# Kernel tuning notes

Measured on AMD Instinct MI355X. Metric: run time of the kernel, lower is better.

The kernel has to match this reference:

```python
import jax, jax.numpy as jnp
import numpy as np

B, S, D, E, H, K = 2, 2048, 1024, 8, 4096, 2


def setup_inputs() -> dict:
    key = jax.random.key(0)
    ks = jax.random.split(key, 8)
    w = lambda i, shape: jax.random.normal(ks[i], shape, jnp.float32) * 0.02
    return {
        "x": jax.random.normal(ks[0], (B, S, D), jnp.float32),
        "noise": jax.random.normal(ks[1], (B, S, E), jnp.float32),
        "Wg": w(2, (E, D)),
        "noise_weight": jnp.zeros((E,), jnp.float32),
        "W1": w(3, (E, D, H)),
        "b1": jnp.zeros((E, H), jnp.float32),
        "W2": w(4, (E, D, H)),
        "b2": jnp.zeros((E, H), jnp.float32),
        "Wp": w(5, (E, H, D)),
        "bp": jnp.zeros((E, D), jnp.float32),
        "k": K,
    }


def reference(x, noise, Wg, noise_weight, W1, b1, W2, b2, Wp, bp, k):
    Bb, Ss, Dd = x.shape
    Ee = Wg.shape[0]
    # --- noisy top-k gate (noisy_std = 1.0) ---
    logits = jnp.einsum('bsd,ed->bse', x, Wg)
    noisy = logits + noise * noise_weight            # [B,S,E]
    vals, idx = jax.lax.top_k(noisy, k)              # [B,S,k]
    oh = jax.nn.one_hot(idx, Ee, dtype=x.dtype)      # [B,S,k,E]
    sel = oh.sum(axis=-2) > 0                        # [B,S,E] selected mask
    scat = (oh * vals[..., None]).sum(axis=-2)       # scatter topk logits
    sparse = jnp.where(sel, scat, -jnp.inf)
    gate = jax.nn.softmax(sparse, axis=-1)           # zero weight off-topk
    # --- dense-equivalent expert compute (gate==0 off top-k => same math as masked dispatch) ---
    xf = x.reshape(Bb * Ss, Dd)                      # [T,D]
    gf = gate.reshape(Bb * Ss, Ee)                   # [T,E]
    h1 = jnp.einsum('td,edh->eth', xf, W1) + b1[:, None, :]
    h2 = jnp.einsum('td,edh->eth', xf, W2) + b2[:, None, :]
    hh = h1 * jax.nn.silu(h2)                        # SwiGLU
    outs = jnp.einsum('eth,ehd->etd', hh, Wp) + bp[:, None, :]
    final = jnp.einsum('etd,te->td', outs, gf).reshape(Bb, Ss, Dd)
    return final, idx
```

## Files before the change

kernel.cpp:

```cpp
#include <hip/hip_runtime.h>
#include <math.h>

#define Bc 2
#define Sc 2048
#define Dc 1024
#define Ec 8
#define Hc 4096
#define Tc (Bc*Sc)
#define NSLOT (Tc*2)
#define SLOTPAD 8448
#define FINAL_N ((size_t)Tc*Dc)
#define BK 32
#define PROWS ((size_t)SLOTPAD*32)

typedef float f32x4 __attribute__((ext_vector_type(4)));
typedef __bf16 bf16x8 __attribute__((ext_vector_type(8)));

__device__ __forceinline__ unsigned short f2bf(float f) {
    union { float f; unsigned int u; } v; v.f = f;
    return (unsigned short)((v.u + 0x7fffu + ((v.u >> 16) & 1u)) >> 16);
}
__device__ __forceinline__ unsigned int pack2bf(float a, float b) {
    return (unsigned int)f2bf(a) | ((unsigned int)f2bf(b) << 16);
}

__device__ __forceinline__ void gload16(const unsigned short* g, unsigned short* l) {
    __builtin_amdgcn_global_load_lds(
        (const __attribute__((address_space(1))) unsigned int*)g,
        (__attribute__((address_space(3))) unsigned int*)l,
        16, 0, 0);
}

__device__ __forceinline__ void fence_bar() {
    __builtin_amdgcn_sched_barrier(0);
    asm volatile("s_barrier" ::: "memory");
    __builtin_amdgcn_sched_barrier(0);
}

__global__ void k_transpose_panel(const float* __restrict__ inA, const float* __restrict__ inB,
                                  unsigned short* __restrict__ outA, unsigned short* __restrict__ outB,
                                  int R, int C, int nz_per_mat) {
    __shared__ float tile[64][65];
    int z = blockIdx.z;
    const float* in; unsigned short* out;
    if (z < nz_per_mat) { in = inA; out = outA; }
    else { in = inB; out = outB; z -= nz_per_mat; }
    size_t zbase = (size_t)z * (size_t)R * C;
    int R32 = R >> 5;
    int cb = blockIdx.x * 64, rb = blockIdx.y * 64;
    int t = threadIdx.x;
    int q = t & 15, g = t >> 4;
    #pragma unroll
    for (int j = 0; j < 4; j++) {
        int row = g + 16*j;
        float4 v = *(const float4*)&in[zbase + (size_t)(rb+row)*C + cb + q*4];
        tile[row][q*4+0] = v.x; tile[row][q*4+1] = v.y;
        tile[row][q*4+2] = v.z; tile[row][q*4+3] = v.w;
    }
    __syncthreads();
    #pragma unroll
    for (int j = 0; j < 4; j++) {
        int co = g + 16*j;
        int c = cb + co;
        int r0 = rb + q*4;
        ushort4 o;
        o.x = f2bf(tile[q*4+0][co]); o.y = f2bf(tile[q*4+1][co]);
        o.z = f2bf(tile[q*4+2][co]); o.w = f2bf(tile[q*4+3][co]);
        int cr = c & 127;
        int ch = ((r0 >> 3) & 3) ^ ((cr >> 1) & 3);
        size_t off = zbase + (((size_t)(c >> 7) * R32 + (r0 >> 5)) * 4096)
                   + (size_t)cr * 32 + ch * 8 + (r0 & 7);
        *(ushort4*)&out[off] = o;
    }
}

__global__ void k_gate(const float* __restrict__ x, const float* __restrict__ noise,
                       const float* __restrict__ Wg, const float* __restrict__ nw,
                       float* __restrict__ out_idx, int* __restrict__ counts,
                       int* __restrict__ tok_top, float* __restrict__ tok_w) {
    int t = blockIdx.x;
    int lane = threadIdx.x;
    const float* xr = x + (size_t)t * Dc;
    double acc[Ec];
    #pragma unroll
    for (int e = 0; e < Ec; e++) acc[e] = 0.0;
    for (int i = 0; i < Dc/64; i++) {
        int d = lane + i*64;
        double xv = (double)xr[d];
        #pragma unroll
        for (int e = 0; e < Ec; e++) acc[e] += xv * (double)Wg[e*Dc + d];
    }
    #pragma unroll
    for (int e = 0; e < Ec; e++)
        for (int off = 32; off > 0; off >>= 1)
            acc[e] += __shfl_down(acc[e], off);
    if (lane == 0) {
        double noisy[Ec];
        #pragma unroll
        for (int e = 0; e < Ec; e++)
            noisy[e] = acc[e] + (double)noise[t*Ec + e] * (double)nw[e];
        int i0 = 0;
        for (int e = 1; e < Ec; e++) if (noisy[e] > noisy[i0]) i0 = e;
        int i1 = -1;
        for (int e = 0; e < Ec; e++) {
            if (e == i0) continue;
            if (i1 < 0 || noisy[e] > noisy[i1]) i1 = e;
        }
        double ee = exp(noisy[i1] - noisy[i0]);
        float w0 = (float)(1.0 / (1.0 + ee));
        float w1 = (float)(ee / (1.0 + ee));
        out_idx[t*2 + 0] = (float)i0;
        out_idx[t*2 + 1] = (float)i1;
        tok_top[t*2] = i0; tok_top[t*2+1] = i1;
        tok_w[t*2] = w0;   tok_w[t*2+1] = w1;
        atomicAdd(&counts[i0], 1);
        atomicAdd(&counts[i1], 1);
    }
}

__global__ void k_scan(const int* __restrict__ counts, int* __restrict__ offsets) {
    if (threadIdx.x == 0) {
        int s = 0;
        for (int e = 0; e < Ec; e++) { offsets[e] = s; s += counts[e]; }
        offsets[Ec] = s;
    }
}

__global__ void k_fill(const int* __restrict__ tok_top, const int* __restrict__ offsets,
                       int* __restrict__ fill, int* __restrict__ slot_token,
                       int* __restrict__ slot_of, int* __restrict__ slot_pos) {
    int t = blockIdx.x * 256 + threadIdx.x;
    if (t >= Tc) return;
    #pragma unroll
    for (int j = 0; j < 2; j++) {
        int e = tok_top[t*2 + j];
        int pos = atomicAdd(&fill[e], 1);
        int slot = offsets[e] + pos;
        slot_token[slot] = t;
        slot_of[t*2 + j] = slot;
        slot_pos[slot] = pos;
    }
}

__global__ void k_packA(const float* __restrict__ x, const int* __restrict__ slot_token,
                        const int* __restrict__ slot_pos, unsigned short* __restrict__ apk) {
    int s = blockIdx.x * 4 + (threadIdx.x >> 6);
    int lane = threadIdx.x & 63;
    int token = slot_token[s];
    int pos = slot_pos[s];
    const float4* px = (const float4*)(x + (size_t)token * Dc) + lane*4;
    float4 v0 = px[0], v1 = px[1], v2 = px[2], v3 = px[3];
    uint4 lo, hi;
    lo.x = pack2bf(v0.x, v0.y); lo.y = pack2bf(v0.z, v0.w);
    lo.z = pack2bf(v1.x, v1.y); lo.w = pack2bf(v1.z, v1.w);
    hi.x = pack2bf(v2.x, v2.y); hi.y = pack2bf(v2.z, v2.w);
    hi.z = pack2bf(v3.x, v3.y); hi.w = pack2bf(v3.z, v3.w);
    int kp = lane >> 1;
    int key = (pos >> 1) & 3;
    int c0 = (lane & 1) * 2;
    size_t base = (size_t)kp * PROWS + (size_t)s * 32;
    *(uint4*)&apk[base + ((c0 ^ key) * 8)]       = lo;
    *(uint4*)&apk[base + (((c0+1) ^ key) * 8)]   = hi;
}

#define BM1 256
#define BN1 128
#define A1SZ (BM1*BK)
#define W1SZ (BN1*BK)

__global__ __launch_bounds__(512, 2) void k_gemm1(
    const unsigned short* __restrict__ apk,
    const unsigned short* __restrict__ w1p, const unsigned short* __restrict__ w2p,
    const float* __restrict__ b1, const float* __restrict__ b2,
    const int* __restrict__ counts, const int* __restrict__ offsets,
    unsigned short* __restrict__ hh2) {
    int e = blockIdx.z;
    int n_e = counts[e];
    int m0 = blockIdx.y * BM1;
    if (m0 >= n_e) return;
    int base = offsets[e];
    int hp = blockIdx.x;
    int n0 = hp * BN1;

    __shared__ __align__(16) unsigned short sA[3*A1SZ];
    __shared__ __align__(16) unsigned short sW1[3*W1SZ];
    __shared__ __align__(16) unsigned short sW2[3*W1SZ];

    int tid = threadIdx.x;
    int wid = tid >> 6, lane = tid & 63;
    int wr = wid >> 1, wc = wid & 1;

    const unsigned short* pa  = apk + (size_t)(base + m0 + wid*32) * 32 + lane*8;
    const unsigned short* pw1 = w1p + ((size_t)(e*32 + hp) * 32) * 4096 + wid*512 + lane*8;
    const unsigned short* pw2 = w2p + ((size_t)(e*32 + hp) * 32) * 4096 + wid*512 + lane*8;

    f32x4 acc1[4][4], acc2[4][4];
    #pragma unroll
    for (int m = 0; m < 4; m++)
        #pragma unroll
        for (int n = 0; n < 4; n++)
            #pragma unroll
            for (int j = 0; j < 4; j++) { acc1[m][n][j] = 0.0f; acc2[m][n][j] = 0.0f; }

    int arow = lane & 15, cr = lane >> 4;
    int ccf = cr ^ ((arow >> 1) & 3);
    int offA[4], offW[4];
    #pragma unroll
    for (int m = 0; m < 4; m++) offA[m] = (wr*64 + m*16 + arow)*BK + ccf*8;
    #pragma unroll
    for (int n = 0; n < 4; n++) offW[n] = (wc*64 + n*16 + arow)*BK + ccf*8;

    auto STAGE = [&](int buf, int kp) {
        unsigned short* dA = sA + buf*A1SZ + wid*1024;
        const unsigned short* a = pa + (size_t)kp * PROWS;
        gload16(a,       dA);
        gload16(a + 512, dA + 512);
        gload16(pw1 + kp*4096, sW1 + buf*W1SZ + wid*512);
        gload16(pw2 + kp*4096, sW2 + buf*W1SZ + wid*512);
    };

#define LDF1(buf, a, w1f, w2f) { \
    const unsigned short* lA_ = sA  + (buf)*A1SZ; \
    const unsigned short* l1_ = sW1 + (buf)*W1SZ; \
    const unsigned short* l2_ = sW2 + (buf)*W1SZ; \
    _Pragma("unroll") for (int m_ = 0; m_ < 4; m_++) a[m_] = *(const bf16x8*)&lA_[offA[m_]]; \
    _Pragma("unroll") for (int n_ = 0; n_ < 4; n_++) { \
        w1f[n_] = *(const bf16x8*)&l1_[offW[n_]]; \
        w2f[n_] = *(const bf16x8*)&l2_[offW[n_]]; } }

#define MM1(a, w1f, w2f) { \
    _Pragma("unroll") for (int m_ = 0; m_ < 4; m_++) \
        _Pragma("unroll") for (int n_ = 0; n_ < 4; n_++) { \
            acc1[m_][n_] = __builtin_amdgcn_mfma_f32_16x16x32_bf16(a[m_], w1f[n_], acc1[m_][n_], 0, 0, 0); \
            acc2[m_][n_] = __builtin_amdgcn_mfma_f32_16x16x32_bf16(a[m_], w2f[n_], acc2[m_][n_], 0, 0, 0); } }

    bf16x8 a0[4], x10[4], x20[4], a1[4], x11[4], x21[4];

    STAGE(0, 0); STAGE(1, 1);
    asm volatile("s_waitcnt vmcnt(4)" ::: "memory");
    fence_bar();
    LDF1(0, a0, x10, x20);
    asm volatile("s_waitcnt lgkmcnt(0)" ::: "memory");
    __builtin_amdgcn_sched_barrier(0);

    const int NT = Dc / BK;
    int ib = 0;

#define G1ITER(T, CA, CW1, CW2, NA, NW1, NW2) { \
    int i1_ = ib + 1; if (i1_ == 3) i1_ = 0; \
    int i2_ = i1_ + 1; if (i2_ == 3) i2_ = 0; \
    if ((T) + 2 < NT) { \
        STAGE(i2_, (T)+2); \
        asm volatile("s_waitcnt vmcnt(4)" ::: "memory");    \
    } else if ((T) + 1 < NT) { \
        asm volatile("s_waitcnt vmcnt(0)" ::: "memory"); \
    } \
    fence_bar();                                 \
    __builtin_amdgcn_s_setprio(1); \
    if ((T) + 1 < NT) LDF1(i1_, NA, NW1, NW2);   \
    MM1(CA, CW1, CW2); \
    __builtin_amdgcn_s_setprio(0); \
    asm volatile("s_waitcnt lgkmcnt(0)" ::: "memory"); \
    __builtin_amdgcn_sched_barrier(0); \
    ib = i1_; }

    for (int t = 0; t < NT; t += 2) {
        G1ITER(t,   a0, x10, x20, a1, x11, x21);
        G1ITER(t+1, a1, x11, x21, a0, x10, x20);
    }

    int lrow = (lane >> 4) * 4, lcol = lane & 15;
    #pragma unroll
    for (int n = 0; n < 4; n++) {
        int hcol = n0 + wc*64 + n*16 + lcol;
        float bias1 = b1[e*Hc + hcol], bias2 = b2[e*Hc + hcol];
        int hp2 = hcol >> 5;
        int ch  = (hcol >> 3) & 3;
        int ho  = hcol & 7;
        #pragma unroll
        for (int m = 0; m < 4; m++) {
            int rb2 = m0 + wr*64 + m*16 + lrow;
            #pragma unroll
            for (int j = 0; j < 4; j++) {
                int r = rb2 + j;
                if (r < n_e) {
                    float h1v = acc1[m][n][j] + bias1;
                    float h2v = acc2[m][n][j] + bias2;
                    float hhv = h1v * (h2v / (1.0f + expf(-h2v)));
                    int key = (r >> 1) & 3;
                    hh2[(size_t)hp2 * PROWS + (size_t)(base + r)*32 + ((ch ^ key)*8) + ho] = f2bf(hhv);
                }
            }
        }
    }
#undef G1ITER
#undef MM1
#undef LDF1
}

#define BM2 256
#define BN2 128
#define A2SZ (BM2*BK)
#define B2SZ (BN2*BK)

__global__ __launch_bounds__(512, 2) void k_gemm2(
    const unsigned short* __restrict__ hh2,
    const unsigned short* __restrict__ wpp,
    const float* __restrict__ bp,
    const int* __restrict__ counts, const int* __restrict__ offsets,
    float* __restrict__ outb) {
    int e = blockIdx.z;
    int n_e = counts[e];
    int m0 = blockIdx.y * BM2;
    if (m0 >= n_e) return;
    int base = offsets[e];
    int dp = blockIdx.x;
    int n0 = dp * BN2;

    __shared__ __align__(16) unsigned short sA[3*A2SZ];
    __shared__ __align__(16) unsigned short sB[3*B2SZ];

    int tid = threadIdx.x;
    int wid = tid >> 6, lane = tid & 63;
    int wr = wid >> 1, wc = wid & 1;

    const unsigned short* pa = hh2 + (size_t)(base + m0 + wid*32) * 32 + lane*8;
    const unsigned short* pb = wpp + ((size_t)(e*8 + dp) * 128) * 4096 + wid*512 + lane*8;

    f32x4 acc[4][4];
    #pragma unroll
    for (int m = 0; m < 4; m++)
        #pragma unroll
        for (int n = 0; n < 4; n++)
            #pragma unroll
            for (int j = 0; j < 4; j++) acc[m][n][j] = 0.0f;

    int arow = lane & 15, cr = lane >> 4;
    int ccf = cr ^ ((arow >> 1) & 3);
    int offA[4], offW[4];
    #pragma unroll
    for (int m = 0; m < 4; m++) offA[m] = (wr*64 + m*16 + arow)*BK + ccf*8;
    #pragma unroll
    for (int n = 0; n < 4; n++) offW[n] = (wc*64 + n*16 + arow)*BK + ccf*8;

    auto STAGE = [&](int buf, int kp) {
        unsigned short* dA = sA + buf*A2SZ + wid*1024;
        const unsigned short* a = pa + (size_t)kp * PROWS;
        gload16(a,       dA);
        gload16(a + 512, dA + 512);
        gload16(pb + kp*4096, sB + buf*B2SZ + wid*512);
    };

#define LDF2(buf, a, b) { \
    const unsigned short* lA_ = sA + (buf)*A2SZ; \
    const unsigned short* lB_ = sB + (buf)*B2SZ; \
    _Pragma("unroll") for (int m_ = 0; m_ < 4; m_++) a[m_] = *(const bf16x8*)&lA_[offA[m_]]; \
    _Pragma("unroll") for (int n_ = 0; n_ < 4; n_++) b[n_] = *(const bf16x8*)&lB_[offW[n_]]; }

#define MM2(a, b) { \
    _Pragma("unroll") for (int m_ = 0; m_ < 4; m_++) \
        _Pragma("unroll") for (int n_ = 0; n_ < 4; n_++) \
            acc[m_][n_] = __builtin_amdgcn_mfma_f32_16x16x32_bf16(a[m_], b[n_], acc[m_][n_], 0, 0, 0); }

    bf16x8 a0[4], b0[4], a1[4], b1f[4];

    STAGE(0, 0); STAGE(1, 1);
    asm volatile("s_waitcnt vmcnt(3)" ::: "memory");
    fence_bar();
    LDF2(0, a0, b0);
    asm volatile("s_waitcnt lgkmcnt(0)" ::: "memory");
    __builtin_amdgcn_sched_barrier(0);

    const int NT = Hc / BK;
    int ib = 0;

#define G2ITER(T, CA, CB, NA, NB) { \
    int i1_ = ib + 1; if (i1_ == 3) i1_ = 0; \
    int i2_ = i1_ + 1; if (i2_ == 3) i2_ = 0; \
    if ((T) + 2 < NT) { \
        STAGE(i2_, (T)+2); \
        asm volatile("s_waitcnt vmcnt(3)" ::: "memory"); \
    } else if ((T) + 1 < NT) { \
        asm volatile("s_waitcnt vmcnt(0)" ::: "memory"); \
    } \
    fence_bar(); \
    __builtin_amdgcn_s_setprio(1); \
    if ((T) + 1 < NT) LDF2(i1_, NA, NB); \
    MM2(CA, CB); \
    __builtin_amdgcn_s_setprio(0); \
    asm volatile("s_waitcnt lgkmcnt(0)" ::: "memory"); \
    __builtin_amdgcn_sched_barrier(0); \
    ib = i1_; }

    for (int t = 0; t < NT; t += 2) {
        G2ITER(t,   a0, b0, a1, b1f);
        G2ITER(t+1, a1, b1f, a0, b0);
    }

    int lrow = (lane >> 4) * 4, lcol = lane & 15;
    #pragma unroll
    for (int n = 0; n < 4; n++) {
        int dcol = n0 + wc*64 + n*16 + lcol;
        float bias = bp[e*Dc + dcol];
        #pragma unroll
        for (int m = 0; m < 4; m++) {
            int rb2 = m0 + wr*64 + m*16 + lrow;
            #pragma unroll
            for (int j = 0; j < 4; j++) {
                int r = rb2 + j;
                if (r < n_e)
                    outb[(size_t)(base + r)*Dc + dcol] = acc[m][n][j] + bias;
            }
        }
    }
#undef G2ITER
#undef MM2
#undef LDF2
}

__global__ void k_combine(const float* __restrict__ outb, const int* __restrict__ slot_of,
                          const float* __restrict__ tok_w, float* __restrict__ final_out) {
    int gid = blockIdx.x * 256 + threadIdx.x;
    int t = gid >> 8;
    int c = (gid & 255) * 4;
    int s0 = slot_of[t*2], s1 = slot_of[t*2 + 1];
    float w0 = tok_w[t*2], w1 = tok_w[t*2 + 1];
    float4 o0 = *(const float4*)&outb[(size_t)s0*Dc + c];
    float4 o1 = *(const float4*)&outb[(size_t)s1*Dc + c];
    float4 r;
    r.x = w0*o0.x + w1*o1.x;
    r.y = w0*o0.y + w1*o1.y;
    r.z = w0*o0.z + w1*o1.z;
    r.w = w0*o0.w + w1*o1.w;
    *(float4*)&final_out[(size_t)t*Dc + c] = r;
}

extern "C" void kernel_launch(void* const* d_in, const int* in_sizes, int n_in,
                              void* d_out, int out_size, void* d_ws, size_t ws_size,
                              hipStream_t stream) {
    (void)in_sizes; (void)n_in; (void)out_size; (void)ws_size;
    const float* x     = (const float*)d_in[0];
    const float* noise = (const float*)d_in[1];
    const float* Wg    = (const float*)d_in[2];
    const float* nw    = (const float*)d_in[3];
    const float* W1    = (const float*)d_in[4];
    const float* b1    = (const float*)d_in[5];
    const float* W2    = (const float*)d_in[6];
    const float* b2    = (const float*)d_in[7];
    const float* Wp    = (const float*)d_in[8];
    const float* bp    = (const float*)d_in[9];

    char* ws = (char*)d_ws;
    size_t off = 0;
    unsigned short* W1P = (unsigned short*)(ws + off); off += (size_t)Ec*Dc*Hc*2;
    unsigned short* W2P = (unsigned short*)(ws + off); off += (size_t)Ec*Dc*Hc*2;
    unsigned short* WPP = (unsigned short*)(ws + off); off += (size_t)Ec*Hc*Dc*2;
    unsigned short* APK = (unsigned short*)(ws + off); off += (size_t)32*PROWS*2;
    unsigned short* HH2 = (unsigned short*)(ws + off); off += (size_t)128*PROWS*2;
    float*          OUTB= (float*)(ws + off);          off += (size_t)NSLOT*Dc*4;
    int*   counts    = (int*)(ws + off);
    int*   fill      = (int*)(ws + off + 32);
    int*   offsets   = (int*)(ws + off + 64);
    int*   tok_top   = (int*)(ws + off + 128);
    float* tok_w     = (float*)(ws + off + 128 + (size_t)Tc*2*4);
    int*   slot_token= (int*)(ws + off + 128 + (size_t)Tc*2*8);
    int*   slot_of   = (int*)(ws + off + 128 + (size_t)Tc*2*8 + (size_t)NSLOT*4);
    int*   slot_pos  = (int*)(ws + off + 128 + (size_t)Tc*2*8 + (size_t)NSLOT*8);

    float* final_out = (float*)d_out;
    float* idx_out   = (float*)d_out + FINAL_N;

    hipMemsetAsync(counts, 0, 64, stream);

    k_transpose_panel<<<dim3(Hc/64, Dc/64, 2*Ec), 256, 0, stream>>>(W1, W2, W1P, W2P, Dc, Hc, Ec);
    k_transpose_panel<<<dim3(Dc/64, Hc/64, Ec), 256, 0, stream>>>(Wp, Wp, WPP, WPP, Hc, Dc, Ec);

    k_gate<<<Tc, 64, 0, stream>>>(x, noise, Wg, nw, idx_out, counts, tok_top, tok_w);
    k_scan<<<1, 64, 0, stream>>>(counts, offsets);
    k_fill<<<Tc/256, 256, 0, stream>>>(tok_top, offsets, fill, slot_token, slot_of, slot_pos);
    k_packA<<<NSLOT/4, 256, 0, stream>>>(x, slot_token, slot_pos, APK);

    k_gemm1<<<dim3(Hc/BN1, Tc/BM1, Ec), 512, 0, stream>>>(APK, W1P, W2P, b1, b2,
                                                          counts, offsets, HH2);
    k_gemm2<<<dim3(Dc/BN2, Tc/BM2, Ec), 512, 0, stream>>>(HH2, WPP, bp, counts, offsets, OUTB);
    k_combine<<<(Tc*Dc/4)/256, 256, 0, stream>>>(OUTB, slot_of, tok_w, final_out);
}
```

Before: 696.9 us.

## Restructure expert GEMM mainloops to BK=64 stages with interleaved sub-phase loads

Both grouped expert GEMMs now stage 64-wide K tiles (two 32-wide panels) per pipeline step. Each step is split into sub-phases that interleave LDS fragment reads, async global-to-LDS loads and MFMA bursts. gemm1 moves to a double-buffered 4x2 wave layout in which each wave covers 128 rows by 32 columns, so only four A fragments are held at a time, lowering register pressure. gemm2 keeps a three-stage ring at the larger K depth. The aim is fewer barriers per unit of K and better overlap of loads with MFMA work; in exchange it adds more fence barriers per step and more LDS, which may hurt occupancy.

```diff
diff --git a/kernel.cpp b/kernel.cpp
--- a/kernel.cpp
+++ b/kernel.cpp
@@ -10,8 +10,9 @@
 #define NSLOT (Tc*2)
 #define SLOTPAD 8448
 #define FINAL_N ((size_t)Tc*Dc)
-#define BK 32
 #define PROWS ((size_t)SLOTPAD*32)
+#define NKT1 16
+#define NKT2 64
 
 typedef float f32x4 __attribute__((ext_vector_type(4)));
 typedef __bf16 bf16x8 __attribute__((ext_vector_type(8)));
@@ -163,11 +164,6 @@
     *(uint4*)&apk[base + (((c0+1) ^ key) * 8)]   = hi;
 }
 
-#define BM1 256
-#define BN1 128
-#define A1SZ (BM1*BK)
-#define W1SZ (BN1*BK)
-
 __global__ __launch_bounds__(512, 2) void k_gemm1(
     const unsigned short* __restrict__ apk,
     const unsigned short* __restrict__ w1p, const unsigned short* __restrict__ w2p,
@@ -176,116 +172,122 @@
     unsigned short* __restrict__ hh2) {
     int e = blockIdx.z;
     int n_e = counts[e];
-    int m0 = blockIdx.y * BM1;
+    int m0 = blockIdx.y * 256;
     if (m0 >= n_e) return;
     int base = offsets[e];
     int hp = blockIdx.x;
-    int n0 = hp * BN1;
-
-    __shared__ __align__(16) unsigned short sA[3*A1SZ];
-    __shared__ __align__(16) unsigned short sW1[3*W1SZ];
-    __shared__ __align__(16) unsigned short sW2[3*W1SZ];
+    int n0 = hp * 128;
+
+    __shared__ __align__(16) unsigned short sA[2][2][8192];
+    __shared__ __align__(16) unsigned short sW1[2][8192];
+    __shared__ __align__(16) unsigned short sW2[2][8192];
 
     int tid = threadIdx.x;
     int wid = tid >> 6, lane = tid & 63;
-    int wr = wid >> 1, wc = wid & 1;
-
-    const unsigned short* pa  = apk + (size_t)(base + m0 + wid*32) * 32 + lane*8;
-    const unsigned short* pw1 = w1p + ((size_t)(e*32 + hp) * 32) * 4096 + wid*512 + lane*8;
-    const unsigned short* pw2 = w2p + ((size_t)(e*32 + hp) * 32) * 4096 + wid*512 + lane*8;
-
-    f32x4 acc1[4][4], acc2[4][4];
-    #pragma unroll
-    for (int m = 0; m < 4; m++)
-        #pragma unroll
-        for (int n = 0; n < 4; n++)
-            #pragma unroll
-            for (int j = 0; j < 4; j++) { acc1[m][n][j] = 0.0f; acc2[m][n][j] = 0.0f; }
+    int wr = wid >> 2, wc = wid & 3;
+
+    const unsigned short* aSrc  = apk + (size_t)(base + m0 + wid*32)*32 + lane*8;
+    const size_t wOff = (size_t)(e*32 + hp) * 32 * 4096;
+    const unsigned short* w1Src = w1p + wOff + wid*1024 + lane*8;
+    const unsigned short* w2Src = w2p + wOff + wid*1024 + lane*8;
 
     int arow = lane & 15, cr = lane >> 4;
     int ccf = cr ^ ((arow >> 1) & 3);
-    int offA[4], offW[4];
-    #pragma unroll
-    for (int m = 0; m < 4; m++) offA[m] = (wr*64 + m*16 + arow)*BK + ccf*8;
-    #pragma unroll
-    for (int n = 0; n < 4; n++) offW[n] = (wc*64 + n*16 + arow)*BK + ccf*8;
-
-    auto STAGE = [&](int buf, int kp) {
-        unsigned short* dA = sA + buf*A1SZ + wid*1024;
-        const unsigned short* a = pa + (size_t)kp * PROWS;
-        gload16(a,       dA);
-        gload16(a + 512, dA + 512);
-        gload16(pw1 + kp*4096, sW1 + buf*W1SZ + wid*512);
-        gload16(pw2 + kp*4096, sW2 + buf*W1SZ + wid*512);
+    int aoff[8], woff[2];
+    #pragma unroll
+    for (int rf = 0; rf < 8; rf++) aoff[rf] = (wr*128 + rf*16 + arow)*32 + ccf*8;
+    #pragma unroll
+    for (int cf = 0; cf < 2; cf++) woff[cf] = (wc*32 + cf*16 + arow)*32 + ccf*8;
+
+    f32x4 acc1[8][2], acc2[8][2];
+    #pragma unroll
+    for (int rf = 0; rf < 8; rf++)
+        #pragma unroll
+        for (int cf = 0; cf < 2; cf++)
+            #pragma unroll
+            for (int j = 0; j < 4; j++) { acc1[rf][cf][j] = 0.0f; acc2[rf][cf][j] = 0.0f; }
+
+    bf16x8 af[4], w1f[2], w2f[2];
+
+    auto ST_W1 = [&](int ss, int kt) {
+        const unsigned short* s_ = w1Src + (size_t)kt*8192;
+        unsigned short* d_ = &sW1[ss][0] + wid*1024;
+        gload16(s_, d_); gload16(s_ + 512, d_ + 512);
     };
-
-#define LDF1(buf, a, w1f, w2f) { \
-    const unsigned short* lA_ = sA  + (buf)*A1SZ; \
-    const unsigned short* l1_ = sW1 + (buf)*W1SZ; \
-    const unsigned short* l2_ = sW2 + (buf)*W1SZ; \
-    _Pragma("unroll") for (int m_ = 0; m_ < 4; m_++) a[m_] = *(const bf16x8*)&lA_[offA[m_]]; \
-    _Pragma("unroll") for (int n_ = 0; n_ < 4; n_++) { \
-        w1f[n_] = *(const bf16x8*)&l1_[offW[n_]]; \
-        w2f[n_] = *(const bf16x8*)&l2_[offW[n_]]; } }
-
-#define MM1(a, w1f, w2f) { \
-    _Pragma("unroll") for (int m_ = 0; m_ < 4; m_++) \
-        _Pragma("unroll") for (int n_ = 0; n_ < 4; n_++) { \
-            acc1[m_][n_] = __builtin_amdgcn_mfma_f32_16x16x32_bf16(a[m_], w1f[n_], acc1[m_][n_], 0, 0, 0); \
-            acc2[m_][n_] = __builtin_amdgcn_mfma_f32_16x16x32_bf16(a[m_], w2f[n_], acc2[m_][n_], 0, 0, 0); } }
-
-    bf16x8 a0[4], x10[4], x20[4], a1[4], x11[4], x21[4];
-
-    STAGE(0, 0); STAGE(1, 1);
-    asm volatile("s_waitcnt vmcnt(4)" ::: "memory");
+    auto ST_W2 = [&](int ss, int kt) {
+        const unsigned short* s_ = w2Src + (size_t)kt*8192;
+        unsigned short* d_ = &sW2[ss][0] + wid*1024;
+        gload16(s_, d_); gload16(s_ + 512, d_ + 512);
+    };
+    auto ST_A = [&](int ss, int p, int kp) {
+        const unsigned short* s_ = aSrc + (size_t)kp*PROWS;
+        unsigned short* d_ = &sA[ss][p][0] + wid*1024;
+        gload16(s_, d_); gload16(s_ + 512, d_ + 512);
+    };
+
+#define LDA1(SLOT, P, RB) { const unsigned short* lA_ = &sA[SLOT][P][0]; \
+    _Pragma("unroll") for (int rf_ = 0; rf_ < 4; rf_++) af[rf_] = *(const bf16x8*)&lA_[aoff[(RB)+rf_]]; }
+#define LDW1(SLOT, P) { const unsigned short* l1_ = &sW1[SLOT][(P)*4096]; \
+    const unsigned short* l2_ = &sW2[SLOT][(P)*4096]; \
+    _Pragma("unroll") for (int cf_ = 0; cf_ < 2; cf_++) { \
+        w1f[cf_] = *(const bf16x8*)&l1_[woff[cf_]]; \
+        w2f[cf_] = *(const bf16x8*)&l2_[woff[cf_]]; } }
+#define MM1P(RB) { __builtin_amdgcn_s_setprio(1); \
+    _Pragma("unroll") for (int rf_ = 0; rf_ < 4; rf_++) \
+        _Pragma("unroll") for (int cf_ = 0; cf_ < 2; cf_++) { \
+            acc1[(RB)+rf_][cf_] = __builtin_amdgcn_mfma_f32_16x16x32_bf16(af[rf_], w1f[cf_], acc1[(RB)+rf_][cf_], 0, 0, 0); \
+            acc2[(RB)+rf_][cf_] = __builtin_amdgcn_mfma_f32_16x16x32_bf16(af[rf_], w2f[cf_], acc2[(RB)+rf_][cf_], 0, 0, 0); } \
+    __builtin_amdgcn_s_setprio(0); }
+
+    ST_W1(0, 0); ST_W2(0, 0); ST_A(0, 0, 0); ST_A(0, 1, 1);
+    asm volatile("s_waitcnt vmcnt(2)" ::: "memory");
     fence_bar();
-    LDF1(0, a0, x10, x20);
-    asm volatile("s_waitcnt lgkmcnt(0)" ::: "memory");
-    __builtin_amdgcn_sched_barrier(0);
-
-    const int NT = Dc / BK;
-    int ib = 0;
-
-#define G1ITER(T, CA, CW1, CW2, NA, NW1, NW2) { \
-    int i1_ = ib + 1; if (i1_ == 3) i1_ = 0; \
-    int i2_ = i1_ + 1; if (i2_ == 3) i2_ = 0; \
-    if ((T) + 2 < NT) { \
-        STAGE(i2_, (T)+2); \
-        asm volatile("s_waitcnt vmcnt(4)" ::: "memory");    \
-    } else if ((T) + 1 < NT) { \
-        asm volatile("s_waitcnt vmcnt(0)" ::: "memory"); \
-    } \
-    fence_bar();                                 \
-    __builtin_amdgcn_s_setprio(1); \
-    if ((T) + 1 < NT) LDF1(i1_, NA, NW1, NW2);   \
-    MM1(CA, CW1, CW2); \
-    __builtin_amdgcn_s_setprio(0); \
-    asm volatile("s_waitcnt lgkmcnt(0)" ::: "memory"); \
-    __builtin_amdgcn_sched_barrier(0); \
-    ib = i1_; }
-
-    for (int t = 0; t < NT; t += 2) {
-        G1ITER(t,   a0, x10, x20, a1, x11, x21);
-        G1ITER(t+1, a1, x11, x21, a0, x10, x20);
+
+    for (int g = 0; g < NKT1; ++g) {
+        int s = g & 1, ss = s ^ 1;
+        bool st = (g + 1 < NKT1);
+        LDA1(s, 0, 0); LDW1(s, 0);
+        if (st) ST_W1(ss, g + 1);
+        fence_bar();
+        MM1P(0);
+        fence_bar();
+        LDA1(s, 0, 4);
+        if (st) ST_W2(ss, g + 1);
+        fence_bar();
+        MM1P(4);
+        if (st) { asm volatile("s_waitcnt vmcnt(4)" ::: "memory"); }
+        else    { asm volatile("s_waitcnt vmcnt(0)" ::: "memory"); }
+        fence_bar();
+        LDA1(s, 1, 0); LDW1(s, 1);
+        if (st) ST_A(ss, 0, 2*(g+1));
+        fence_bar();
+        MM1P(0);
+        fence_bar();
+        LDA1(s, 1, 4);
+        if (st) ST_A(ss, 1, 2*(g+1) + 1);
+        fence_bar();
+        MM1P(4);
+        if (st) { asm volatile("s_waitcnt vmcnt(2)" ::: "memory"); }
+        fence_bar();
     }
 
     int lrow = (lane >> 4) * 4, lcol = lane & 15;
     #pragma unroll
-    for (int n = 0; n < 4; n++) {
-        int hcol = n0 + wc*64 + n*16 + lcol;
+    for (int cf = 0; cf < 2; cf++) {
+        int hcol = n0 + wc*32 + cf*16 + lcol;
         float bias1 = b1[e*Hc + hcol], bias2 = b2[e*Hc + hcol];
         int hp2 = hcol >> 5;
         int ch  = (hcol >> 3) & 3;
         int ho  = hcol & 7;
         #pragma unroll
-        for (int m = 0; m < 4; m++) {
-            int rb2 = m0 + wr*64 + m*16 + lrow;
+        for (int rf = 0; rf < 8; rf++) {
+            int rb2 = m0 + wr*128 + rf*16 + lrow;
             #pragma unroll
             for (int j = 0; j < 4; j++) {
                 int r = rb2 + j;
                 if (r < n_e) {
-                    float h1v = acc1[m][n][j] + bias1;
-                    float h2v = acc2[m][n][j] + bias2;
+                    float h1v = acc1[rf][cf][j] + bias1;
+                    float h2v = acc2[rf][cf][j] + bias2;
                     float hhv = h1v * (h2v / (1.0f + expf(-h2v)));
                     int key = (r >> 1) & 3;
                     hh2[(size_t)hp2 * PROWS + (size_t)(base + r)*32 + ((ch ^ key)*8) + ho] = f2bf(hhv);
@@ -293,15 +295,10 @@
             }
         }
     }
-#undef G1ITER
-#undef MM1
-#undef LDF1
-}
-
-#define BM2 256
-#define BN2 128
-#define A2SZ (BM2*BK)
-#define B2SZ (BN2*BK)
+#undef LDA1
+#undef LDW1
+#undef MM1P
+}
 
 __global__ __launch_bounds__(512, 2) void k_gemm2(
     const unsigned short* __restrict__ hh2,
@@ -311,111 +308,103 @@
     float* __restrict__ outb) {
     int e = blockIdx.z;
     int n_e = counts[e];
-    int m0 = blockIdx.y * BM2;
+    int m0 = blockIdx.y * 256;
     if (m0 >= n_e) return;
     int base = offsets[e];
     int dp = blockIdx.x;
-    int n0 = dp * BN2;
-
-    __shared__ __align__(16) unsigned short sA[3*A2SZ];
-    __shared__ __align__(16) unsigned short sB[3*B2SZ];
+    int n0 = dp * 128;
+
+    __shared__ __align__(16) unsigned short sA2[3][2][8192];
+    __shared__ __align__(16) unsigned short sB2[3][8192];
 
     int tid = threadIdx.x;
     int wid = tid >> 6, lane = tid & 63;
     int wr = wid >> 1, wc = wid & 1;
 
-    const unsigned short* pa = hh2 + (size_t)(base + m0 + wid*32) * 32 + lane*8;
-    const unsigned short* pb = wpp + ((size_t)(e*8 + dp) * 128) * 4096 + wid*512 + lane*8;
-
-    f32x4 acc[4][4];
-    #pragma unroll
-    for (int m = 0; m < 4; m++)
-        #pragma unroll
-        for (int n = 0; n < 4; n++)
-            #pragma unroll
-            for (int j = 0; j < 4; j++) acc[m][n][j] = 0.0f;
+    const unsigned short* aSrc = hh2 + (size_t)(base + m0 + wid*32)*32 + lane*8;
+    const unsigned short* bSrc = wpp + (size_t)e*Hc*Dc + (size_t)dp*128*4096
+                                     + wid*1024 + lane*8;
 
     int arow = lane & 15, cr = lane >> 4;
     int ccf = cr ^ ((arow >> 1) & 3);
-    int offA[4], offW[4];
-    #pragma unroll
-    for (int m = 0; m < 4; m++) offA[m] = (wr*64 + m*16 + arow)*BK + ccf*8;
-    #pragma unroll
-    for (int n = 0; n < 4; n++) offW[n] = (wc*64 + n*16 + arow)*BK + ccf*8;
-
-    auto STAGE = [&](int buf, int kp) {
-        unsigned short* dA = sA + buf*A2SZ + wid*1024;
-        const unsigned short* a = pa + (size_t)kp * PROWS;
-        gload16(a,       dA);
-        gload16(a + 512, dA + 512);
-        gload16(pb + kp*4096, sB + buf*B2SZ + wid*512);
+    int aoff[4], boff[4];
+    #pragma unroll
+    for (int rf = 0; rf < 4; rf++) aoff[rf] = (wr*64 + rf*16 + arow)*32 + ccf*8;
+    #pragma unroll
+    for (int cf = 0; cf < 4; cf++) boff[cf] = (wc*64 + cf*16 + arow)*32 + ccf*8;
+
+    f32x4 acc[4][4];
+    #pragma unroll
+    for (int rf = 0; rf < 4; rf++)
+        #pragma unroll
+        for (int cf = 0; cf < 4; cf++)
+            #pragma unroll
+            for (int j = 0; j < 4; j++) acc[rf][cf][j] = 0.0f;
+
+    bf16x8 af[4], bf[4];
+
+    auto ST_A2 = [&](int ss, int p, int kp) {
+        const unsigned short* s_ = aSrc + (size_t)kp*PROWS;
+        unsigned short* d_ = &sA2[ss][p][0] + wid*1024;
+        gload16(s_, d_); gload16(s_ + 512, d_ + 512);
     };
-
-#define LDF2(buf, a, b) { \
-    const unsigned short* lA_ = sA + (buf)*A2SZ; \
-    const unsigned short* lB_ = sB + (buf)*B2SZ; \
-    _Pragma("unroll") for (int m_ = 0; m_ < 4; m_++) a[m_] = *(const bf16x8*)&lA_[offA[m_]]; \
-    _Pragma("unroll") for (int n_ = 0; n_ < 4; n_++) b[n_] = *(const bf16x8*)&lB_[offW[n_]]; }
-
-#define MM2(a, b) { \
-    _Pragma("unroll") for (int m_ = 0; m_ < 4; m_++) \
-        _Pragma("unroll") for (int n_ = 0; n_ < 4; n_++) \
-            acc[m_][n_] = __builtin_amdgcn_mfma_f32_16x16x32_bf16(a[m_], b[n_], acc[m_][n_], 0, 0, 0); }
-
-    bf16x8 a0[4], b0[4], a1[4], b1f[4];
-
-    STAGE(0, 0); STAGE(1, 1);
-    asm volatile("s_waitcnt vmcnt(3)" ::: "memory");
+    auto ST_B2 = [&](int ss, int kt) {
+        const unsigned short* s_ = bSrc + (size_t)kt*8192;
+        unsigned short* d_ = &sB2[ss][0] + wid*1024;
+        gload16(s_, d_); gload16(s_ + 512, d_ + 512);
+    };
+
+#define LDA2(SLOT, P) { const unsigned short* lA_ = &sA2[SLOT][P][0]; \
+    _Pragma("unroll") for (int rf_ = 0; rf_ < 4; rf_++) af[rf_] = *(const bf16x8*)&lA_[aoff[rf_]]; }
+#define LDB2(SLOT, P) { const unsigned short* lB_ = &sB2[SLOT][(P)*4096]; \
+    _Pragma("unroll") for (int cf_ = 0; cf_ < 4; cf_++) bf[cf_] = *(const bf16x8*)&lB_[boff[cf_]]; }
+#define MM2P() { __builtin_amdgcn_s_setprio(1); \
+    _Pragma("unroll") for (int rf_ = 0; rf_ < 4; rf_++) \
+        _Pragma("unroll") for (int cf_ = 0; cf_ < 4; cf_++) \
+            acc[rf_][cf_] = __builtin_amdgcn_mfma_f32_16x16x32_bf16(af[rf_], bf[cf_], acc[rf_][cf_], 0, 0, 0); \
+    __builtin_amdgcn_s_setprio(0); }
+
+    ST_A2(0, 0, 0); ST_A2(0, 1, 1); ST_B2(0, 0);
+    ST_A2(1, 0, 2); ST_A2(1, 1, 3); ST_B2(1, 1);
+    asm volatile("s_waitcnt vmcnt(6)" ::: "memory");
     fence_bar();
-    LDF2(0, a0, b0);
-    asm volatile("s_waitcnt lgkmcnt(0)" ::: "memory");
-    __builtin_amdgcn_sched_barrier(0);
-
-    const int NT = Hc / BK;
-    int ib = 0;
-
-#define G2ITER(T, CA, CB, NA, NB) { \
-    int i1_ = ib + 1; if (i1_ == 3) i1_ = 0; \
-    int i2_ = i1_ + 1; if (i2_ == 3) i2_ = 0; \
-    if ((T) + 2 < NT) { \
-        STAGE(i2_, (T)+2); \
-        asm volatile("s_waitcnt vmcnt(3)" ::: "memory"); \
-    } else if ((T) + 1 < NT) { \
-        asm volatile("s_waitcnt vmcnt(0)" ::: "memory"); \
-    } \
-    fence_bar(); \
-    __builtin_amdgcn_s_setprio(1); \
-    if ((T) + 1 < NT) LDF2(i1_, NA, NB); \
-    MM2(CA, CB); \
-    __builtin_amdgcn_s_setprio(0); \
-    asm volatile("s_waitcnt lgkmcnt(0)" ::: "memory"); \
-    __builtin_amdgcn_sched_barrier(0); \
-    ib = i1_; }
-
-    for (int t = 0; t < NT; t += 2) {
-        G2ITER(t,   a0, b0, a1, b1f);
-        G2ITER(t+1, a1, b1f, a0, b0);
+
+    for (int j = 0; j < NKT2; ++j) {
+        int s = j % 3, ss = (j + 2) % 3;
+        bool st = (j + 2 < NKT2);
+        LDA2(s, 0); LDB2(s, 0);
+        if (st) { ST_A2(ss, 0, 2*(j+2)); ST_A2(ss, 1, 2*(j+2) + 1); }
+        fence_bar();
+        MM2P();
+        fence_bar();
+        LDA2(s, 1); LDB2(s, 1);
+        if (st) ST_B2(ss, j + 2);
+        fence_bar();
+        MM2P();
+        if (st)                   { asm volatile("s_waitcnt vmcnt(6)" ::: "memory"); }
+        else if (j + 1 < NKT2)    { asm volatile("s_waitcnt vmcnt(0)" ::: "memory"); }
+        fence_bar();
     }
 
     int lrow = (lane >> 4) * 4, lcol = lane & 15;
     #pragma unroll
-    for (int n = 0; n < 4; n++) {
-        int dcol = n0 + wc*64 + n*16 + lcol;
+    for (int cf = 0; cf < 4; cf++) {
+        int dcol = n0 + wc*64 + cf*16 + lcol;
         float bias = bp[e*Dc + dcol];
         #pragma unroll
-        for (int m = 0; m < 4; m++) {
-            int rb2 = m0 + wr*64 + m*16 + lrow;
+        for (int rf = 0; rf < 4; rf++) {
+            int rb2 = m0 + wr*64 + rf*16 + lrow;
             #pragma unroll
             for (int j = 0; j < 4; j++) {
                 int r = rb2 + j;
                 if (r < n_e)
-                    outb[(size_t)(base + r)*Dc + dcol] = acc[m][n][j] + bias;
+                    outb[(size_t)(base + r)*Dc + dcol] = acc[rf][cf][j] + bias;
             }
         }
     }
-#undef G2ITER
-#undef MM2
-#undef LDF2
+#undef LDA2
+#undef LDB2
+#undef MM2P
 }
 
 __global__ void k_combine(const float* __restrict__ outb, const int* __restrict__ slot_of,
@@ -480,8 +469,8 @@
     k_fill<<<Tc/256, 256, 0, stream>>>(tok_top, offsets, fill, slot_token, slot_of, slot_pos);
     k_packA<<<NSLOT/4, 256, 0, stream>>>(x, slot_token, slot_pos, APK);
 
-    k_gemm1<<<dim3(Hc/BN1, Tc/BM1, Ec), 512, 0, stream>>>(APK, W1P, W2P, b1, b2,
+    k_gemm1<<<dim3(Hc/128, Tc/256, Ec), 512, 0, stream>>>(APK, W1P, W2P, b1, b2,
                                                           counts, offsets, HH2);
-    k_gemm2<<<dim3(Dc/BN2, Tc/BM2, Ec), 512, 0, stream>>>(HH2, WPP, bp, counts, offsets, OUTB);
+    k_gemm2<<<dim3(Dc/128, Tc/256, Ec), 512, 0, stream>>>(HH2, WPP, bp, counts, offsets, OUTB);
     k_combine<<<(Tc*Dc/4)/256, 256, 0, stream>>>(OUTB, slot_of, tok_w, final_out);
 }
```

Result: slower. 711.5 us (+2.1%).

## Replace pipelined large-tile expert GEMMs with simple single-buffered 128x128 tiles

Applied to the files above, without the earlier changes.

Both expert GEMMs drop the triple-buffered, manually scheduled 256x128 tiles (512 threads) for a plain single-buffered loop over 128-row tiles with 256 threads and __syncthreads around each K step. gemm1 now computes W1 and W2 halves in separate waves and combines them through shared memory for the SwiGLU epilogue. This raises occupancy and cuts register and LDS use, but removes the load/compute overlap and doubles the barriers per K step.

```diff
diff --git a/kernel.cpp b/kernel.cpp
--- a/kernel.cpp
+++ b/kernel.cpp
@@ -10,7 +10,6 @@
 #define NSLOT (Tc*2)
 #define SLOTPAD 8448
 #define FINAL_N ((size_t)Tc*Dc)
-#define BK 32
 #define PROWS ((size_t)SLOTPAD*32)
 
 typedef float f32x4 __attribute__((ext_vector_type(4)));
@@ -29,12 +28,6 @@
         (const __attribute__((address_space(1))) unsigned int*)g,
         (__attribute__((address_space(3))) unsigned int*)l,
         16, 0, 0);
-}
-
-__device__ __forceinline__ void fence_bar() {
-    __builtin_amdgcn_sched_barrier(0);
-    asm volatile("s_barrier" ::: "memory");
-    __builtin_amdgcn_sched_barrier(0);
 }
 
 __global__ void k_transpose_panel(const float* __restrict__ inA, const float* __restrict__ inB,
@@ -163,12 +156,7 @@
     *(uint4*)&apk[base + (((c0+1) ^ key) * 8)]   = hi;
 }
 
-#define BM1 256
-#define BN1 128
-#define A1SZ (BM1*BK)
-#define W1SZ (BN1*BK)
-
-__global__ __launch_bounds__(512, 2) void k_gemm1(
+__global__ __launch_bounds__(256, 4) void k_gemm1(
     const unsigned short* __restrict__ apk,
     const unsigned short* __restrict__ w1p, const unsigned short* __restrict__ w2p,
     const float* __restrict__ b1, const float* __restrict__ b2,
@@ -176,134 +164,109 @@
     unsigned short* __restrict__ hh2) {
     int e = blockIdx.z;
     int n_e = counts[e];
-    int m0 = blockIdx.y * BM1;
+    int m0 = blockIdx.y * 128;
     if (m0 >= n_e) return;
     int base = offsets[e];
-    int hp = blockIdx.x;
-    int n0 = hp * BN1;
-
-    __shared__ __align__(16) unsigned short sA[3*A1SZ];
-    __shared__ __align__(16) unsigned short sW1[3*W1SZ];
-    __shared__ __align__(16) unsigned short sW2[3*W1SZ];
+    int bx = blockIdx.x;
+    int n0 = bx * 64;
+    int hp = bx >> 1, ro = (bx & 1) * 64;
+
+    __shared__ __align__(16) unsigned char smem[32768];
+    unsigned short* sA = (unsigned short*)smem;
+    unsigned short* sB = (unsigned short*)(smem + 16384);
+    float* sS = (float*)smem;
 
     int tid = threadIdx.x;
     int wid = tid >> 6, lane = tid & 63;
     int wr = wid >> 1, wc = wid & 1;
 
-    const unsigned short* pa  = apk + (size_t)(base + m0 + wid*32) * 32 + lane*8;
-    const unsigned short* pw1 = w1p + ((size_t)(e*32 + hp) * 32) * 4096 + wid*512 + lane*8;
-    const unsigned short* pw2 = w2p + ((size_t)(e*32 + hp) * 32) * 4096 + wid*512 + lane*8;
-
-    f32x4 acc1[4][4], acc2[4][4];
-    #pragma unroll
-    for (int m = 0; m < 4; m++)
-        #pragma unroll
-        for (int n = 0; n < 4; n++)
-            #pragma unroll
-            for (int j = 0; j < 4; j++) { acc1[m][n][j] = 0.0f; acc2[m][n][j] = 0.0f; }
+    const unsigned short* aSrc = apk + (size_t)(base + m0 + wid*32)*32 + lane*8;
+    const unsigned short* wmat = (wid < 2) ? w1p : w2p;
+    const unsigned short* bSrc = wmat + ((size_t)(e*32 + hp) * 32) * 4096
+                               + (size_t)(ro + (wid & 1)*32)*32 + lane*8;
 
     int arow = lane & 15, cr = lane >> 4;
     int ccf = cr ^ ((arow >> 1) & 3);
-    int offA[4], offW[4];
-    #pragma unroll
-    for (int m = 0; m < 4; m++) offA[m] = (wr*64 + m*16 + arow)*BK + ccf*8;
-    #pragma unroll
-    for (int n = 0; n < 4; n++) offW[n] = (wc*64 + n*16 + arow)*BK + ccf*8;
-
-    auto STAGE = [&](int buf, int kp) {
-        unsigned short* dA = sA + buf*A1SZ + wid*1024;
-        const unsigned short* a = pa + (size_t)kp * PROWS;
-        gload16(a,       dA);
-        gload16(a + 512, dA + 512);
-        gload16(pw1 + kp*4096, sW1 + buf*W1SZ + wid*512);
-        gload16(pw2 + kp*4096, sW2 + buf*W1SZ + wid*512);
-    };
-
-#define LDF1(buf, a, w1f, w2f) { \
-    const unsigned short* lA_ = sA  + (buf)*A1SZ; \
-    const unsigned short* l1_ = sW1 + (buf)*W1SZ; \
-    const unsigned short* l2_ = sW2 + (buf)*W1SZ; \
-    _Pragma("unroll") for (int m_ = 0; m_ < 4; m_++) a[m_] = *(const bf16x8*)&lA_[offA[m_]]; \
-    _Pragma("unroll") for (int n_ = 0; n_ < 4; n_++) { \
-        w1f[n_] = *(const bf16x8*)&l1_[offW[n_]]; \
-        w2f[n_] = *(const bf16x8*)&l2_[offW[n_]]; } }
-
-#define MM1(a, w1f, w2f) { \
-    _Pragma("unroll") for (int m_ = 0; m_ < 4; m_++) \
-        _Pragma("unroll") for (int n_ = 0; n_ < 4; n_++) { \
-            acc1[m_][n_] = __builtin_amdgcn_mfma_f32_16x16x32_bf16(a[m_], w1f[n_], acc1[m_][n_], 0, 0, 0); \
-            acc2[m_][n_] = __builtin_amdgcn_mfma_f32_16x16x32_bf16(a[m_], w2f[n_], acc2[m_][n_], 0, 0, 0); } }
-
-    bf16x8 a0[4], x10[4], x20[4], a1[4], x11[4], x21[4];
-
-    STAGE(0, 0); STAGE(1, 1);
-    asm volatile("s_waitcnt vmcnt(4)" ::: "memory");
-    fence_bar();
-    LDF1(0, a0, x10, x20);
-    asm volatile("s_waitcnt lgkmcnt(0)" ::: "memory");
-    __builtin_amdgcn_sched_barrier(0);
-
-    const int NT = Dc / BK;
-    int ib = 0;
-
-#define G1ITER(T, CA, CW1, CW2, NA, NW1, NW2) { \
-    int i1_ = ib + 1; if (i1_ == 3) i1_ = 0; \
-    int i2_ = i1_ + 1; if (i2_ == 3) i2_ = 0; \
-    if ((T) + 2 < NT) { \
-        STAGE(i2_, (T)+2); \
-        asm volatile("s_waitcnt vmcnt(4)" ::: "memory");    \
-    } else if ((T) + 1 < NT) { \
-        asm volatile("s_waitcnt vmcnt(0)" ::: "memory"); \
-    } \
-    fence_bar();                                 \
-    __builtin_amdgcn_s_setprio(1); \
-    if ((T) + 1 < NT) LDF1(i1_, NA, NW1, NW2);   \
-    MM1(CA, CW1, CW2); \
-    __builtin_amdgcn_s_setprio(0); \
-    asm volatile("s_waitcnt lgkmcnt(0)" ::: "memory"); \
-    __builtin_amdgcn_sched_barrier(0); \
-    ib = i1_; }
-
-    for (int t = 0; t < NT; t += 2) {
-        G1ITER(t,   a0, x10, x20, a1, x11, x21);
-        G1ITER(t+1, a1, x11, x21, a0, x10, x20);
+    int aoff[4], boff[4];
+    #pragma unroll
+    for (int m = 0; m < 4; m++) aoff[m] = (wr*64 + m*16 + arow)*32 + ccf*8;
+    #pragma unroll
+    for (int n = 0; n < 4; n++) boff[n] = (wc*64 + n*16 + arow)*32 + ccf*8;
+
+    f32x4 acc[4][4];
+    #pragma unroll
+    for (int m = 0; m < 4; m++)
+        #pragma unroll
+        for (int n = 0; n < 4; n++)
+            #pragma unroll
+            for (int j = 0; j < 4; j++) acc[m][n][j] = 0.0f;
+
+    unsigned short* dA = sA + wid*1024;
+    unsigned short* dB = sB + wid*1024;
+
+    const int NK = Dc / 32;
+    for (int kk = 0; kk < NK; ++kk) {
+        const unsigned short* a = aSrc + (size_t)kk*PROWS;
+        const unsigned short* b = bSrc + (size_t)kk*4096;
+        gload16(a,       dA); gload16(a + 512, dA + 512);
+        gload16(b,       dB); gload16(b + 512, dB + 512);
+        __syncthreads();
+        bf16x8 af[4], bf[4];
+        #pragma unroll
+        for (int m = 0; m < 4; m++) af[m] = *(const bf16x8*)&sA[aoff[m]];
+        #pragma unroll
+        for (int n = 0; n < 4; n++) bf[n] = *(const bf16x8*)&sB[boff[n]];
+        #pragma unroll
+        for (int m = 0; m < 4; m++)
+            #pragma unroll
+            for (int n = 0; n < 4; n++)
+                acc[m][n] = __builtin_amdgcn_mfma_f32_16x16x32_bf16(af[m], bf[n], acc[m][n], 0, 0, 0);
+        __syncthreads();
     }
 
     int lrow = (lane >> 4) * 4, lcol = lane & 15;
-    #pragma unroll
-    for (int n = 0; n < 4; n++) {
-        int hcol = n0 + wc*64 + n*16 + lcol;
-        float bias1 = b1[e*Hc + hcol], bias2 = b2[e*Hc + hcol];
-        int hp2 = hcol >> 5;
-        int ch  = (hcol >> 3) & 3;
-        int ho  = hcol & 7;
-        #pragma unroll
-        for (int m = 0; m < 4; m++) {
-            int rb2 = m0 + wr*64 + m*16 + lrow;
-            #pragma unroll
-            for (int j = 0; j < 4; j++) {
-                int r = rb2 + j;
-                if (r < n_e) {
-                    float h1v = acc1[m][n][j] + bias1;
-                    float h2v = acc2[m][n][j] + bias2;
-                    float hhv = h1v * (h2v / (1.0f + expf(-h2v)));
-                    int key = (r >> 1) & 3;
-                    hh2[(size_t)hp2 * PROWS + (size_t)(base + r)*32 + ((ch ^ key)*8) + ho] = f2bf(hhv);
+    if (wc == 1) {
+        #pragma unroll
+        for (int n = 0; n < 4; n++) {
+            float b2v = b2[e*Hc + n0 + n*16 + lcol];
+            #pragma unroll
+            for (int m = 0; m < 4; m++) {
+                int rb = wr*64 + m*16 + lrow;
+                #pragma unroll
+                for (int j = 0; j < 4; j++) {
+                    float h2 = acc[m][n][j] + b2v;
+                    sS[(rb + j)*64 + n*16 + lcol] = h2 / (1.0f + expf(-h2));
                 }
             }
         }
     }
-#undef G1ITER
-#undef MM1
-#undef LDF1
-}
-
-#define BM2 256
-#define BN2 128
-#define A2SZ (BM2*BK)
-#define B2SZ (BN2*BK)
-
-__global__ __launch_bounds__(512, 2) void k_gemm2(
+    __syncthreads();
+    if (wc == 0) {
+        #pragma unroll
+        for (int n = 0; n < 4; n++) {
+            int hcol = n0 + n*16 + lcol;
+            float b1v = b1[e*Hc + hcol];
+            int hp2 = hcol >> 5;
+            int ch  = (hcol >> 3) & 3;
+            int ho  = hcol & 7;
+            #pragma unroll
+            for (int m = 0; m < 4; m++) {
+                int rb = wr*64 + m*16 + lrow;
+                #pragma unroll
+                for (int j = 0; j < 4; j++) {
+                    int r = m0 + rb + j;
+                    if (r < n_e) {
+                        float v = (acc[m][n][j] + b1v) * sS[(rb + j)*64 + n*16 + lcol];
+                        int key = (r >> 1) & 3;
+                        hh2[(size_t)hp2 * PROWS + (size_t)(base + r)*32 + ((ch ^ key)*8) + ho] = f2bf(v);
+                    }
+                }
+            }
+        }
+    }
+}
+
+__global__ __launch_bounds__(256, 4) void k_gemm2(
     const unsigned short* __restrict__ hh2,
     const unsigned short* __restrict__ wpp,
     const float* __restrict__ bp,
@@ -311,90 +274,60 @@
     float* __restrict__ outb) {
     int e = blockIdx.z;
     int n_e = counts[e];
-    int m0 = blockIdx.y * BM2;
+    int m0 = blockIdx.y * 128;
     if (m0 >= n_e) return;
     int base = offsets[e];
     int dp = blockIdx.x;
-    int n0 = dp * BN2;
-
-    __shared__ __align__(16) unsigned short sA[3*A2SZ];
-    __shared__ __align__(16) unsigned short sB[3*B2SZ];
+    int n0 = dp * 128;
+
+    __shared__ __align__(16) unsigned short sA[128*32];
+    __shared__ __align__(16) unsigned short sB[128*32];
 
     int tid = threadIdx.x;
     int wid = tid >> 6, lane = tid & 63;
     int wr = wid >> 1, wc = wid & 1;
 
-    const unsigned short* pa = hh2 + (size_t)(base + m0 + wid*32) * 32 + lane*8;
-    const unsigned short* pb = wpp + ((size_t)(e*8 + dp) * 128) * 4096 + wid*512 + lane*8;
-
-    f32x4 acc[4][4];
-    #pragma unroll
-    for (int m = 0; m < 4; m++)
-        #pragma unroll
-        for (int n = 0; n < 4; n++)
-            #pragma unroll
-            for (int j = 0; j < 4; j++) acc[m][n][j] = 0.0f;
+    const unsigned short* aSrc = hh2 + (size_t)(base + m0 + wid*32)*32 + lane*8;
+    const unsigned short* bSrc = wpp + ((size_t)(e*8 + dp) * 128) * 4096
+                               + wid*1024 + lane*8;
 
     int arow = lane & 15, cr = lane >> 4;
     int ccf = cr ^ ((arow >> 1) & 3);
-    int offA[4], offW[4];
-    #pragma unroll
-    for (int m = 0; m < 4; m++) offA[m] = (wr*64 + m*16 + arow)*BK + ccf*8;
-    #pragma unroll
-    for (int n = 0; n < 4; n++) offW[n] = (wc*64 + n*16 + arow)*BK + ccf*8;
-
-    auto STAGE = [&](int buf, int kp) {
-        unsigned short* dA = sA + buf*A2SZ + wid*1024;
-        const unsigned short* a = pa + (size_t)kp * PROWS;
-        gload16(a,       dA);
-        gload16(a + 512, dA + 512);
-        gload16(pb + kp*4096, sB + buf*B2SZ + wid*512);
-    };
-
-#define LDF2(buf, a, b) { \
-    const unsigned short* lA_ = sA + (buf)*A2SZ; \
-    const unsigned short* lB_ = sB + (buf)*B2SZ; \
-    _Pragma("unroll") for (int m_ = 0; m_ < 4; m_++) a[m_] = *(const bf16x8*)&lA_[offA[m_]]; \
-    _Pragma("unroll") for (int n_ = 0; n_ < 4; n_++) b[n_] = *(const bf16x8*)&lB_[offW[n_]]; }
-
-#define MM2(a, b) { \
-    _Pragma("unroll") for (int m_ = 0; m_ < 4; m_++) \
-        _Pragma("unroll") for (int n_ = 0; n_ < 4; n_++) \
-            acc[m_][n_] = __builtin_amdgcn_mfma_f32_16x16x32_bf16(a[m_], b[n_], acc[m_][n_], 0, 0, 0); }
-
-    bf16x8 a0[4], b0[4], a1[4], b1f[4];
-
-    STAGE(0, 0); STAGE(1, 1);
-    asm volatile("s_waitcnt vmcnt(3)" ::: "memory");
-    fence_bar();
-    LDF2(0, a0, b0);
-    asm volatile("s_waitcnt lgkmcnt(0)" ::: "memory");
-    __builtin_amdgcn_sched_barrier(0);
-
-    const int NT = Hc / BK;
-    int ib = 0;
-
-#define G2ITER(T, CA, CB, NA, NB) { \
-    int i1_ = ib + 1; if (i1_ == 3) i1_ = 0; \
-    int i2_ = i1_ + 1; if (i2_ == 3) i2_ = 0; \
-    if ((T) + 2 < NT) { \
-        STAGE(i2_, (T)+2); \
-        asm volatile("s_waitcnt vmcnt(3)" ::: "memory"); \
-    } else if ((T) + 1 < NT) { \
-        asm volatile("s_waitcnt vmcnt(0)" ::: "memory"); \
-    } \
-    fence_bar(); \
-    __builtin_amdgcn_s_setprio(1); \
-    if ((T) + 1 < NT) LDF2(i1_, NA, NB); \
-    MM2(CA, CB); \
-    __builtin_amdgcn_s_setprio(0); \
-    asm volatile("s_waitcnt lgkmcnt(0)" ::: "memory"); \
-    __builtin_amdgcn_sched_barrier(0); \
-    ib = i1_; }
-
-    for (int t = 0; t < NT; t += 2) {
-        G2ITER(t,   a0, b0, a1, b1f);
-        G2ITER(t+1, a1, b1f, a0, b0);
+    int aoff[4], boff[4];
+    #pragma unroll
+    for (int m = 0; m < 4; m++) aoff[m] = (wr*64 + m*16 + arow)*32 + ccf*8;
+    #pragma unroll
+    for (int n = 0; n < 4; n++) boff[n] = (wc*64 + n*16 + arow)*32 + ccf*8;
+
+    f32x4 acc[4][4];
+    #pragma unroll
+    for (int m = 0; m < 4; m++)
+        #pragma unroll
+        for (int n = 0; n < 4; n++)
+            #pragma unroll
+            for (int j = 0; j < 4; j++) acc[m][n][j] = 0.0f;
+
+    unsigned short* dA = sA + wid*1024;
+    unsigned short* dB = sB + wid*1024;
+
+    const int NK = Hc / 32;
+    for (int kk = 0; kk < NK; ++kk) {
+        const unsigned short* a = aSrc + (size_t)kk*PROWS;
+        const unsigned short* b = bSrc + (size_t)kk*4096;
+        gload16(a,       dA); gload16(a + 512, dA + 512);
+        gload16(b,       dB); gload16(b + 512, dB + 512);
+        __syncthreads();
+        bf16x8 af[4], bf[4];
+        #pragma unroll
+        for (int m = 0; m < 4; m++) af[m] = *(const bf16x8*)&sA[aoff[m]];
+        #pragma unroll
+        for (int n = 0; n < 4; n++) bf[n] = *(const bf16x8*)&sB[boff[n]];
+        #pragma unroll
+        for (int m = 0; m < 4; m++)
+            #pragma unroll
+            for (int n = 0; n < 4; n++)
+                acc[m][n] = __builtin_amdgcn_mfma_f32_16x16x32_bf16(af[m], bf[n], acc[m][n], 0, 0, 0);
+        __syncthreads();
     }
 
     int lrow = (lane >> 4) * 4, lcol = lane & 15;
@@ -413,9 +346,6 @@
             }
         }
     }
-#undef G2ITER
-#undef MM2
-#undef LDF2
 }
 
 __global__ void k_combine(const float* __restrict__ outb, const int* __restrict__ slot_of,
@@ -480,8 +410,8 @@
     k_fill<<<Tc/256, 256, 0, stream>>>(tok_top, offsets, fill, slot_token, slot_of, slot_pos);
     k_packA<<<NSLOT/4, 256, 0, stream>>>(x, slot_token, slot_pos, APK);
 
-    k_gemm1<<<dim3(Hc/BN1, Tc/BM1, Ec), 512, 0, stream>>>(APK, W1P, W2P, b1, b2,
-                                                          counts, offsets, HH2);
-    k_gemm2<<<dim3(Dc/BN2, Tc/BM2, Ec), 512, 0, stream>>>(HH2, WPP, bp, counts, offsets, OUTB);
+    k_gemm1<<<dim3(Hc/64, Tc/128, Ec), 256, 0, stream>>>(APK, W1P, W2P, b1, b2,
+                                                         counts, offsets, HH2);
+    k_gemm2<<<dim3(Dc/128, Tc/128, Ec), 256, 0, stream>>>(HH2, WPP, bp, counts, offsets, OUTB);
     k_combine<<<(Tc*Dc/4)/256, 256, 0, stream>>>(OUTB, slot_of, tok_w, final_out);
 }
```

Result: faster. 660.0 us (-5.3%).
